# Kernel tuning notes

Measured on AMD Instinct MI355X. Metric: run time of the kernel, lower is better.

## Reference

```python
import jax, jax.numpy as jnp
import numpy as np

H = 1024      # hidden_dim
NH = 16       # num_heads
HD = H // NH  # head_dim
EPS = 1e-12
SCALE = float(np.sqrt(H))


def setup_inputs() -> dict:
    key = jax.random.key(0)
    ks = jax.random.split(key, 12)
    S, B = 2048, 2
    inp = {
        "query": jax.random.normal(ks[0], (S, B, 2 * H), jnp.float32),
        "key":   jax.random.normal(ks[1], (S, B, H), jnp.float32),
        "value": jax.random.normal(ks[2], (S, B, H), jnp.float32),
        # gating params (zeros in torch init, but randomize for a meaningful test)
        "qs": jax.random.normal(ks[3], (1, 1, H), jnp.float32) * 0.02,
        "ks_p": jax.random.normal(ks[4], (1, 1, H), jnp.float32) * 0.02,
        "vs": jax.random.normal(ks[5], (1, 1, H), jnp.float32) * 0.02,
        # Overparam vq: Linear(H, 2H)
        "vq_w": jax.random.normal(ks[6], (2 * H, H), jnp.float32) * (1.0 / np.sqrt(H)),
        "vq_b": jax.random.normal(ks[7], (2 * H,), jnp.float32) * 0.02,
        # q_linear: Linear(2H, H)
        "ql_w": jax.random.normal(ks[8], (H, 2 * H), jnp.float32) * (1.0 / np.sqrt(2 * H)),
        "ql_b": jax.random.normal(ks[9], (H,), jnp.float32) * 0.02,
        # LayerNorm(H)
        "ln_g": jnp.ones((H,), jnp.float32),
        "ln_b": jnp.zeros((H,), jnp.float32),
    }
    return inp


def _layernorm(x, g, b):
    mu = jnp.mean(x, axis=-1, keepdims=True)
    var = jnp.mean(jnp.square(x - mu), axis=-1, keepdims=True)
    return (x - mu) * jax.lax.rsqrt(var + EPS) * g + b


def reference(query, key, value, qs, ks_p, vs, vq_w, vq_b, ql_w, ql_b, ln_g, ln_b):
    # gate vectors
    qsig = jax.nn.sigmoid(qs)            # [1,1,H]
    ksig = jax.nn.sigmoid(ks_p)          # [1,1,H]
    # vq = Overparam(sigmoid(vs)): c,f = l1(x).split(H); sigmoid(f)*tanh(c)
    h = jax.nn.sigmoid(vs) @ vq_w.T + vq_b   # [1,1,2H]
    c, f = h[..., :H], h[..., H:]
    vsig = jax.nn.sigmoid(f) * jnp.tanh(c)   # [1,1,H]

    q = qsig * _layernorm(query @ ql_w.T + ql_b, ln_g, ln_b)  # [S,B,H]
    k = ksig * key
    v = vsig * value

    # batch-first
    q = jnp.transpose(q, (1, 0, 2))  # [B,Q,H]
    k = jnp.transpose(k, (1, 0, 2))  # [B,K,H]
    v = jnp.transpose(v, (1, 0, 2))
    B, Q, _ = q.shape
    K = k.shape[1]

    qh = q.reshape(B, Q, NH, HD)
    kh = k.reshape(B, K, NH, HD)
    vh = v.reshape(B, K, NH, HD)

    scores = jnp.einsum('bqhd,bkhd->bhqk', qh, kh) / SCALE
    w = jax.nn.softmax(scores, axis=-1)                # [B,NH,Q,K]
    out = jnp.einsum('bhqk,bkhd->bqhd', w, vh).reshape(B, Q, H)
    # torch code's final .transpose(0,1) is not assigned -> output is [Q,B,H]
    return jnp.transpose(out, (1, 0, 2))
```

## Files before the change

kernel.cpp:

```cpp
#include <hip/hip_runtime.h>

typedef __bf16 bf16x8 __attribute__((ext_vector_type(8)));
typedef float f32x4 __attribute__((ext_vector_type(4)));
typedef unsigned short u16x8 __attribute__((ext_vector_type(8)));
typedef unsigned short u16x4 __attribute__((ext_vector_type(4)));
typedef unsigned short u16;
typedef unsigned int u32;


__device__ __forceinline__ float b2f(u16 u) {
  union { unsigned int i; float f; } x; x.i = ((unsigned int)u) << 16; return x.f;
}
__device__ __forceinline__ u16 f2b(float f) {
  union { float f; unsigned int i; } x; x.f = f;
  unsigned int r = (x.i + 0x7fffu + ((x.i >> 16) & 1u)) >> 16;
  return (u16)r;
}
__device__ __forceinline__ float sigm(float x) { return 1.0f / (1.0f + __expf(-x)); }

__device__ __forceinline__ void async16(u16* lds, const u16* g) {
  __builtin_amdgcn_global_load_lds((const __attribute__((address_space(1))) void*)g,
                                   (__attribute__((address_space(3))) void*)lds, 16, 0, 0);
}

__global__ __launch_bounds__(256) void k_cvt_all(const float4* __restrict__ q, u16x4* __restrict__ qd,
                                                 const float4* __restrict__ w, u16x4* __restrict__ wd,
                                                 const float4* __restrict__ k, u16x4* __restrict__ kd,
                                                 const float4* __restrict__ v, u16x4* __restrict__ vd) {
  int b = blockIdx.x;
  const float4* s; u16x4* d; int i;
  if (b < 8192)       { s = q; d = qd; i = b * 256 + threadIdx.x; }
  else if (b < 10240) { s = w; d = wd; i = (b - 8192) * 256 + threadIdx.x; }
  else if (b < 14336) { s = k; d = kd; i = (b - 10240) * 256 + threadIdx.x; }
  else                { s = v; d = vd; i = (b - 14336) * 256 + threadIdx.x; }
  float4 x = s[i];
  u16x4 o; o[0] = f2b(x.x); o[1] = f2b(x.y); o[2] = f2b(x.z); o[3] = f2b(x.w);
  d[i] = o;
}

__global__ __launch_bounds__(256) void k_h(const float* __restrict__ vs,
                                           const float* __restrict__ vq_w,
                                           const float* __restrict__ vq_b,
                                           float* __restrict__ h) {
  __shared__ float svs[1024];
  int t = threadIdx.x;
  for (int i = t; i < 1024; i += 256) svs[i] = sigm(vs[i]);
  __syncthreads();
  int wave = t >> 6, lane = t & 63;
  int row = blockIdx.x * 4 + wave;
  const float4* w4 = (const float4*)(vq_w + (size_t)row * 1024);
  const float4* s4 = (const float4*)svs;
  float acc = 0.f;
#pragma unroll
  for (int k = 0; k < 4; ++k) {
    float4 w = w4[k * 64 + lane];
    float4 s = s4[k * 64 + lane];
    acc += w.x * s.x + w.y * s.y + w.z * s.z + w.w * s.w;
  }
#pragma unroll
  for (int off = 1; off < 64; off <<= 1) acc += __shfl_xor(acc, off);
  if (lane == 0) h[row] = acc + vq_b[row];
}

__global__ __launch_bounds__(256) void k_scales(const float* __restrict__ h,
                                                const float* __restrict__ qs,
                                                const float* __restrict__ ks,
                                                float* __restrict__ qk_scale,
                                                float* __restrict__ vsig) {
  int ch = blockIdx.x * 256 + threadIdx.x;
  qk_scale[ch] = sigm(qs[ch]) * sigm(ks[ch]) * (1.0f / 32.0f);
  float c = h[ch], f = h[1024 + ch];
  vsig[ch] = sigm(f) * tanhf(c);
}

__global__ __launch_bounds__(256) void k_gemm(const u16* __restrict__ A,
                                              const u16* __restrict__ Bt,
                                              u16* __restrict__ C) {
  __shared__ __align__(16) u16 As[128 * 32];
  __shared__ __align__(16) u16 Bs[128 * 32];
  int tid = threadIdx.x;
  int wave = tid >> 6, lane = tid & 63;
  int l15 = lane & 15, quad = lane >> 4;
  int bx = blockIdx.x & 255;
  int kh = blockIdx.x >> 8;
  int kofs = kh << 10;
  int m0 = (bx >> 3) * 128;
  int n0 = (bx & 7) * 128;
  int wm = (wave >> 1) * 64, wn = (wave & 1) * 64;
  f32x4 acc[4][4] = {};
  int c1 = tid, c2 = tid + 256;
  const u16* ga1 = A + (size_t)(m0 + (c1 >> 2)) * 2048 + kofs + (c1 & 3) * 8;
  const u16* ga2 = A + (size_t)(m0 + (c2 >> 2)) * 2048 + kofs + (c2 & 3) * 8;
  const u16* gb1 = Bt + (size_t)(n0 + (c1 >> 2)) * 2048 + kofs + (c1 & 3) * 8;
  const u16* gb2 = Bt + (size_t)(n0 + (c2 >> 2)) * 2048 + kofs + (c2 & 3) * 8;
  u16* lA1 = As + wave * 512;
  u16* lA2 = As + 2048 + wave * 512;
  u16* lB1 = Bs + wave * 512;
  u16* lB2 = Bs + 2048 + wave * 512;
  for (int kt = 0; kt < 32; ++kt) {
    async16(lA1, ga1); async16(lA2, ga2);
    async16(lB1, gb1); async16(lB2, gb2);
    ga1 += 32; ga2 += 32; gb1 += 32; gb2 += 32;
    __syncthreads();
    bf16x8 af[4], bfr[4];
#pragma unroll
    for (int mt = 0; mt < 4; ++mt)
      af[mt] = *(const bf16x8*)(As + (wm + mt * 16 + l15) * 32 + quad * 8);
#pragma unroll
    for (int nt = 0; nt < 4; ++nt)
      bfr[nt] = *(const bf16x8*)(Bs + (wn + nt * 16 + l15) * 32 + quad * 8);
#pragma unroll
    for (int mt = 0; mt < 4; ++mt)
#pragma unroll
      for (int nt = 0; nt < 4; ++nt)
        acc[mt][nt] = __builtin_amdgcn_mfma_f32_16x16x32_bf16(af[mt], bfr[nt], acc[mt][nt], 0, 0, 0);
    __syncthreads();
  }
  u16* Cp = C + (size_t)kh * 4096 * 1024;
#pragma unroll
  for (int mt = 0; mt < 4; ++mt) {
#pragma unroll
    for (int r = 0; r < 4; ++r) {
      int m = m0 + wm + mt * 16 + quad * 4 + r;
      u16* crow = Cp + (size_t)m * 1024 + n0 + wn + l15;
#pragma unroll
      for (int nt = 0; nt < 4; ++nt) crow[nt * 16] = f2b(acc[mt][nt][r]);
    }
  }
}

__global__ __launch_bounds__(256) void k_ln(const u16* __restrict__ qpre0,
                                            const u16* __restrict__ qpre1,
                                            const float* __restrict__ ql_b,
                                            const float* __restrict__ ln_g,
                                            const float* __restrict__ ln_b,
                                            const float* __restrict__ qk_scale,
                                            u16* __restrict__ qatt) {
  int row = blockIdx.x;
  int t = threadIdx.x;
  u16x4 a4 = *(const u16x4*)(qpre0 + (size_t)row * 1024 + t * 4);
  u16x4 b4 = *(const u16x4*)(qpre1 + (size_t)row * 1024 + t * 4);
  float v[4];
  float s = 0.f, ss = 0.f;
#pragma unroll
  for (int j = 0; j < 4; ++j) {
    v[j] = b2f(a4[j]) + b2f(b4[j]) + ql_b[t * 4 + j];
    s += v[j]; ss += v[j] * v[j];
  }
#pragma unroll
  for (int off = 1; off < 64; off <<= 1) { s += __shfl_xor(s, off); ss += __shfl_xor(ss, off); }
  __shared__ float red[8];
  int wv = t >> 6, ln = t & 63;
  if (ln == 0) { red[wv] = s; red[4 + wv] = ss; }
  __syncthreads();
  s = red[0] + red[1] + red[2] + red[3];
  ss = red[4] + red[5] + red[6] + red[7];
  float mu = s * (1.f / 1024.f);
  float rstd = rsqrtf(ss * (1.f / 1024.f) - mu * mu + 1e-12f);
  int sidx = row >> 1, b = row & 1;
  int ch0 = t * 4;
  int hh = ch0 >> 6, hd0 = ch0 & 63;
  u16* dst = qatt + ((size_t)(b * 16 + hh) * 2048 + sidx) * 64 + hd0;
#pragma unroll
  for (int j = 0; j < 4; ++j) {
    int ch = ch0 + j;
    float y = (v[j] - mu) * rstd * ln_g[ch] + ln_b[ch];
    dst[j] = f2b(y * qk_scale[ch]);
  }
}

__global__ __launch_bounds__(256, 4) void k_attn(const u16* __restrict__ qatt,
                                                 const u16* __restrict__ key,
                                                 const u16* __restrict__ value,
                                                 const float* __restrict__ vsig,
                                                 float* __restrict__ out) {
  int bh = blockIdx.x & 31;
  int qt = blockIdx.x >> 5;
  int b = bh >> 4, h = bh & 15;
  int tid = threadIdx.x, wave = tid >> 6, lane = tid & 63;
  int l15 = lane & 15, quad = lane >> 4;
  int q0 = qt * 64;

  __shared__ __align__(16) u16 Kt[64 * 72];
  __shared__ __align__(16) u16 Vt[2][64 * 72];
  __shared__ __align__(16) u16 Pb[4][16 * 72];

  const u16* qrow = qatt + ((size_t)bh * 2048 + q0 + wave * 16 + l15) * 64 + quad * 8;
  bf16x8 qf0 = *(const bf16x8*)qrow;
  bf16x8 qf1 = *(const bf16x8*)(qrow + 32);

  const u16* kb = key + (size_t)b * 1024 + (size_t)h * 64;
  const u16* vb = value + (size_t)b * 1024 + (size_t)h * 64;
  u16* Pw = Pb[wave];

  int p = lane & 31;
  int chalf = lane >> 5;
  int chbase = wave * 16 + chalf * 8;
  const u16* vsrc = vb + (size_t)2 * p * 2048 + chbase;

  int krow = wave * 16 + (lane >> 3);
  int kch  = (lane & 7) * 8;
  const u16* ksrc = kb + (size_t)krow * 2048 + kch;
  u16* kdst = Kt + krow * 72 + kch;

  {
    u16x8 k0 = *(const u16x8*)ksrc;
    u16x8 k1 = *(const u16x8*)(ksrc + (size_t)8 * 2048);
    *(u16x8*)kdst = k0;
    *(u16x8*)(kdst + 8 * 72) = k1;
    u16x8 va = *(const u16x8*)vsrc;
    u16x8 vbq = *(const u16x8*)(vsrc + 2048);
#pragma unroll
    for (int c = 0; c < 8; ++c) {
      u32 pk = (u32)va[c] | ((u32)vbq[c] << 16);
      *(u32*)(&Vt[0][(chbase + c) * 72 + 2 * p]) = pk;
    }
  }
  __syncthreads();

  f32x4 oacc[4] = {};
  float l_i[4] = {0.f, 0.f, 0.f, 0.f};

  for (int kt = 0; kt < 32; ++kt) {
    int cur = kt & 1;
    f32x4 sacc[4] = {};
#pragma unroll
    for (int nt = 0; nt < 4; ++nt) {
      const u16* kr = Kt + (nt * 16 + l15) * 72 + quad * 8;
      bf16x8 kfa = *(const bf16x8*)kr;
      bf16x8 kfb = *(const bf16x8*)(kr + 32);
      sacc[nt] = __builtin_amdgcn_mfma_f32_16x16x32_bf16(qf0, kfa, sacc[nt], 0, 0, 0);
      sacc[nt] = __builtin_amdgcn_mfma_f32_16x16x32_bf16(qf1, kfb, sacc[nt], 0, 0, 0);
    }
    u16x8 pk0, pk1, va, vbq;
    if (kt < 31) {
      const u16* ks2 = ksrc + (size_t)(kt + 1) * 64 * 2048;
      pk0 = *(const u16x8*)ks2;
      pk1 = *(const u16x8*)(ks2 + (size_t)8 * 2048);
      const u16* vs2 = vsrc + (size_t)(kt + 1) * 64 * 2048;
      va = *(const u16x8*)vs2;
      vbq = *(const u16x8*)(vs2 + 2048);
    }
#pragma unroll
    for (int r = 0; r < 4; ++r) {
      float p0 = __expf(sacc[0][r]);
      float p1 = __expf(sacc[1][r]);
      float p2 = __expf(sacc[2][r]);
      float p3 = __expf(sacc[3][r]);
      l_i[r] += (p0 + p1) + (p2 + p3);
      u16* prow = Pw + (quad * 4 + r) * 72 + l15;
      prow[0]  = f2b(p0);
      prow[16] = f2b(p1);
      prow[32] = f2b(p2);
      prow[48] = f2b(p3);
    }
    bf16x8 pf0 = *(const bf16x8*)(Pw + l15 * 72 + quad * 8);
    bf16x8 pf1 = *(const bf16x8*)(Pw + l15 * 72 + 32 + quad * 8);
    const u16* vt = Vt[cur];
#pragma unroll
    for (int nt = 0; nt < 4; ++nt) {
      int ch = nt * 16 + l15;
      bf16x8 vf0 = *(const bf16x8*)(vt + ch * 72 + quad * 8);
      bf16x8 vf1 = *(const bf16x8*)(vt + ch * 72 + 32 + quad * 8);
      oacc[nt] = __builtin_amdgcn_mfma_f32_16x16x32_bf16(pf0, vf0, oacc[nt], 0, 0, 0);
      oacc[nt] = __builtin_amdgcn_mfma_f32_16x16x32_bf16(pf1, vf1, oacc[nt], 0, 0, 0);
    }
    __syncthreads();
    if (kt < 31) {
      *(u16x8*)kdst = pk0;
      *(u16x8*)(kdst + 8 * 72) = pk1;
      u16* vd = Vt[cur ^ 1];
#pragma unroll
      for (int c = 0; c < 8; ++c) {
        u32 pk = (u32)va[c] | ((u32)vbq[c] << 16);
        *(u32*)(&vd[(chbase + c) * 72 + 2 * p]) = pk;
      }
    }
    __syncthreads();
  }
#pragma unroll
  for (int r = 0; r < 4; ++r) {
    float l = l_i[r];
    l += __shfl_xor(l, 1);
    l += __shfl_xor(l, 2);
    l += __shfl_xor(l, 4);
    l += __shfl_xor(l, 8);
    l_i[r] = l;
  }
#pragma unroll
  for (int r = 0; r < 4; ++r) {
    int sq = q0 + wave * 16 + quad * 4 + r;
    float inv = 1.0f / l_i[r];
    float* orow = out + ((size_t)sq * 2 + b) * 1024 + h * 64;
#pragma unroll
    for (int nt = 0; nt < 4; ++nt) {
      int ch = nt * 16 + l15;
      orow[ch] = oacc[nt][r] * inv * vsig[h * 64 + ch];
    }
  }
}

extern "C" void kernel_launch(void* const* d_in, const int* in_sizes, int n_in,
                              void* d_out, int out_size, void* d_ws, size_t ws_size,
                              hipStream_t stream) {
  (void)in_sizes; (void)n_in; (void)out_size; (void)ws_size;
  const float* query = (const float*)d_in[0];
  const float* key   = (const float*)d_in[1];
  const float* value = (const float*)d_in[2];
  const float* qs    = (const float*)d_in[3];
  const float* ksp   = (const float*)d_in[4];
  const float* vs    = (const float*)d_in[5];
  const float* vq_w  = (const float*)d_in[6];
  const float* vq_b  = (const float*)d_in[7];
  const float* ql_w  = (const float*)d_in[8];
  const float* ql_b  = (const float*)d_in[9];
  const float* ln_g  = (const float*)d_in[10];
  const float* ln_b  = (const float*)d_in[11];
  float* out = (float*)d_out;

  float* ws = (float*)d_ws;
  float* h        = ws;
  float* qk_scale = ws + 2048;
  float* vsig     = ws + 3072;
  u16* qpre  = (u16*)(ws + 4096);
  u16* qbf   = qpre + (size_t)2 * 4096 * 1024;
  u16* qatt  = qbf;
  u16* wbf   = qbf + (size_t)4096 * 2048;
  u16* kbf   = wbf + (size_t)1024 * 2048;
  u16* vbf   = kbf + (size_t)4096 * 1024;

  hipLaunchKernelGGL(k_cvt_all, dim3(18432), dim3(256), 0, stream,
                     (const float4*)query, (u16x4*)qbf,
                     (const float4*)ql_w,  (u16x4*)wbf,
                     (const float4*)key,   (u16x4*)kbf,
                     (const float4*)value, (u16x4*)vbf);
  hipLaunchKernelGGL(k_h,      dim3(512),  dim3(256), 0, stream, vs, vq_w, vq_b, h);
  hipLaunchKernelGGL(k_scales, dim3(4),    dim3(256), 0, stream, h, qs, ksp, qk_scale, vsig);
  hipLaunchKernelGGL(k_gemm,   dim3(512),  dim3(256), 0, stream, qbf, wbf, qpre);
  hipLaunchKernelGGL(k_ln,     dim3(4096), dim3(256), 0, stream, qpre, qpre + (size_t)4096 * 1024,
                     ql_b, ln_g, ln_b, qk_scale, qatt);
  hipLaunchKernelGGL(k_attn,   dim3(1024), dim3(256), 0, stream, qatt, kbf, vbf, vsig, out);
}
```

Measured before the change: 244.2 us.

## Double query tile per attention block, double-buffer K, use exp2, drop scales kernel

Each attention block now handles 128 query rows (two 16-row fragments per wave), so every K/V tile staged in LDS is reused across twice as many queries. The grid is halved and occupancy is lowered to 2 blocks per CU. K is now double-buffered, which removes one barrier per iteration, and the log2(e) factor is folded into the query gate so softmax can use the native exp2. The separate k_scales kernel is removed: gates are computed inline in k_ln and the value gate in the attention epilogue. This trades more registers, LDS and fewer blocks for fewer LDS loads, fewer barriers and one fewer launch.

```diff
diff --git a/kernel.cpp b/kernel.cpp
--- a/kernel.cpp
+++ b/kernel.cpp
@@ -7,6 +7,8 @@
 typedef unsigned short u16;
 typedef unsigned int u32;
 
+
+#define LOG2E 1.4426950408889634f
 
 __device__ __forceinline__ float b2f(u16 u) {
   union { unsigned int i; float f; } x; x.i = ((unsigned int)u) << 16; return x.f;
@@ -60,17 +62,6 @@
 #pragma unroll
   for (int off = 1; off < 64; off <<= 1) acc += __shfl_xor(acc, off);
   if (lane == 0) h[row] = acc + vq_b[row];
-}
-
-__global__ __launch_bounds__(256) void k_scales(const float* __restrict__ h,
-                                                const float* __restrict__ qs,
-                                                const float* __restrict__ ks,
-                                                float* __restrict__ qk_scale,
-                                                float* __restrict__ vsig) {
-  int ch = blockIdx.x * 256 + threadIdx.x;
-  qk_scale[ch] = sigm(qs[ch]) * sigm(ks[ch]) * (1.0f / 32.0f);
-  float c = h[ch], f = h[1024 + ch];
-  vsig[ch] = sigm(f) * tanhf(c);
 }
 
 __global__ __launch_bounds__(256) void k_gemm(const u16* __restrict__ A,
@@ -134,7 +125,8 @@
                                             const float* __restrict__ ql_b,
                                             const float* __restrict__ ln_g,
                                             const float* __restrict__ ln_b,
-                                            const float* __restrict__ qk_scale,
+                                            const float* __restrict__ qs,
+                                            const float* __restrict__ ks,
                                             u16* __restrict__ qatt) {
   int row = blockIdx.x;
   int t = threadIdx.x;
@@ -164,73 +156,80 @@
 #pragma unroll
   for (int j = 0; j < 4; ++j) {
     int ch = ch0 + j;
+    float gate = sigm(qs[ch]) * sigm(ks[ch]) * (LOG2E / 32.0f);
     float y = (v[j] - mu) * rstd * ln_g[ch] + ln_b[ch];
-    dst[j] = f2b(y * qk_scale[ch]);
-  }
-}
-
-__global__ __launch_bounds__(256, 4) void k_attn(const u16* __restrict__ qatt,
+    dst[j] = f2b(y * gate);
+  }
+}
+
+__global__ __launch_bounds__(256, 2) void k_attn(const u16* __restrict__ qatt,
                                                  const u16* __restrict__ key,
                                                  const u16* __restrict__ value,
-                                                 const float* __restrict__ vsig,
+                                                 const float* __restrict__ hbuf,
                                                  float* __restrict__ out) {
   int bh = blockIdx.x & 31;
   int qt = blockIdx.x >> 5;
   int b = bh >> 4, h = bh & 15;
   int tid = threadIdx.x, wave = tid >> 6, lane = tid & 63;
   int l15 = lane & 15, quad = lane >> 4;
-  int q0 = qt * 64;
-
-  __shared__ __align__(16) u16 Kt[64 * 72];
+  int q0 = qt * 128;
+
+  __shared__ __align__(16) u16 Kt[2][64 * 72];
   __shared__ __align__(16) u16 Vt[2][64 * 72];
-  __shared__ __align__(16) u16 Pb[4][16 * 72];
-
-  const u16* qrow = qatt + ((size_t)bh * 2048 + q0 + wave * 16 + l15) * 64 + quad * 8;
-  bf16x8 qf0 = *(const bf16x8*)qrow;
-  bf16x8 qf1 = *(const bf16x8*)(qrow + 32);
+  __shared__ __align__(16) u16 Pb[4][32 * 72];
+
+  bf16x8 qf[2][2];
+#pragma unroll
+  for (int f = 0; f < 2; ++f) {
+    const u16* qrow = qatt + ((size_t)bh * 2048 + q0 + f * 64 + wave * 16 + l15) * 64 + quad * 8;
+    qf[f][0] = *(const bf16x8*)qrow;
+    qf[f][1] = *(const bf16x8*)(qrow + 32);
+  }
 
   const u16* kb = key + (size_t)b * 1024 + (size_t)h * 64;
   const u16* vb = value + (size_t)b * 1024 + (size_t)h * 64;
   u16* Pw = Pb[wave];
 
   int p = lane & 31;
-  int chalf = lane >> 5;
-  int chbase = wave * 16 + chalf * 8;
+  int chbase = wave * 16 + (lane >> 5) * 8;
   const u16* vsrc = vb + (size_t)2 * p * 2048 + chbase;
-
   int krow = wave * 16 + (lane >> 3);
   int kch  = (lane & 7) * 8;
   const u16* ksrc = kb + (size_t)krow * 2048 + kch;
-  u16* kdst = Kt + krow * 72 + kch;
+  int kdofs = krow * 72 + kch;
+  int vdofs_base = 2 * p;
 
   {
     u16x8 k0 = *(const u16x8*)ksrc;
     u16x8 k1 = *(const u16x8*)(ksrc + (size_t)8 * 2048);
-    *(u16x8*)kdst = k0;
-    *(u16x8*)(kdst + 8 * 72) = k1;
+    *(u16x8*)(&Kt[0][kdofs]) = k0;
+    *(u16x8*)(&Kt[0][kdofs + 8 * 72]) = k1;
     u16x8 va = *(const u16x8*)vsrc;
     u16x8 vbq = *(const u16x8*)(vsrc + 2048);
 #pragma unroll
     for (int c = 0; c < 8; ++c) {
       u32 pk = (u32)va[c] | ((u32)vbq[c] << 16);
-      *(u32*)(&Vt[0][(chbase + c) * 72 + 2 * p]) = pk;
+      *(u32*)(&Vt[0][(chbase + c) * 72 + vdofs_base]) = pk;
     }
   }
   __syncthreads();
 
-  f32x4 oacc[4] = {};
-  float l_i[4] = {0.f, 0.f, 0.f, 0.f};
+  f32x4 oacc[2][4] = {};
+  float l_i[2][4] = {};
 
   for (int kt = 0; kt < 32; ++kt) {
     int cur = kt & 1;
-    f32x4 sacc[4] = {};
+    f32x4 sacc[2][4] = {};
+    const u16* ktc = Kt[cur];
 #pragma unroll
     for (int nt = 0; nt < 4; ++nt) {
-      const u16* kr = Kt + (nt * 16 + l15) * 72 + quad * 8;
+      const u16* kr = ktc + (nt * 16 + l15) * 72 + quad * 8;
       bf16x8 kfa = *(const bf16x8*)kr;
       bf16x8 kfb = *(const bf16x8*)(kr + 32);
-      sacc[nt] = __builtin_amdgcn_mfma_f32_16x16x32_bf16(qf0, kfa, sacc[nt], 0, 0, 0);
-      sacc[nt] = __builtin_amdgcn_mfma_f32_16x16x32_bf16(qf1, kfb, sacc[nt], 0, 0, 0);
+      sacc[0][nt] = __builtin_amdgcn_mfma_f32_16x16x32_bf16(qf[0][0], kfa, sacc[0][nt], 0, 0, 0);
+      sacc[0][nt] = __builtin_amdgcn_mfma_f32_16x16x32_bf16(qf[0][1], kfb, sacc[0][nt], 0, 0, 0);
+      sacc[1][nt] = __builtin_amdgcn_mfma_f32_16x16x32_bf16(qf[1][0], kfa, sacc[1][nt], 0, 0, 0);
+      sacc[1][nt] = __builtin_amdgcn_mfma_f32_16x16x32_bf16(qf[1][1], kfb, sacc[1][nt], 0, 0, 0);
     }
     u16x8 pk0, pk1, va, vbq;
     if (kt < 31) {
@@ -242,62 +241,79 @@
       vbq = *(const u16x8*)(vs2 + 2048);
     }
 #pragma unroll
-    for (int r = 0; r < 4; ++r) {
-      float p0 = __expf(sacc[0][r]);
-      float p1 = __expf(sacc[1][r]);
-      float p2 = __expf(sacc[2][r]);
-      float p3 = __expf(sacc[3][r]);
-      l_i[r] += (p0 + p1) + (p2 + p3);
-      u16* prow = Pw + (quad * 4 + r) * 72 + l15;
-      prow[0]  = f2b(p0);
-      prow[16] = f2b(p1);
-      prow[32] = f2b(p2);
-      prow[48] = f2b(p3);
-    }
-    bf16x8 pf0 = *(const bf16x8*)(Pw + l15 * 72 + quad * 8);
-    bf16x8 pf1 = *(const bf16x8*)(Pw + l15 * 72 + 32 + quad * 8);
+    for (int f = 0; f < 2; ++f) {
+#pragma unroll
+      for (int r = 0; r < 4; ++r) {
+        float p0 = __builtin_amdgcn_exp2f(sacc[f][0][r]);
+        float p1 = __builtin_amdgcn_exp2f(sacc[f][1][r]);
+        float p2 = __builtin_amdgcn_exp2f(sacc[f][2][r]);
+        float p3 = __builtin_amdgcn_exp2f(sacc[f][3][r]);
+        l_i[f][r] += (p0 + p1) + (p2 + p3);
+        u16* prow = Pw + (f * 16 + quad * 4 + r) * 72 + l15;
+        prow[0]  = f2b(p0);
+        prow[16] = f2b(p1);
+        prow[32] = f2b(p2);
+        prow[48] = f2b(p3);
+      }
+    }
+    bf16x8 pf[2][2];
+#pragma unroll
+    for (int f = 0; f < 2; ++f) {
+      pf[f][0] = *(const bf16x8*)(Pw + (f * 16 + l15) * 72 + quad * 8);
+      pf[f][1] = *(const bf16x8*)(Pw + (f * 16 + l15) * 72 + 32 + quad * 8);
+    }
     const u16* vt = Vt[cur];
 #pragma unroll
     for (int nt = 0; nt < 4; ++nt) {
-      int ch = nt * 16 + l15;
-      bf16x8 vf0 = *(const bf16x8*)(vt + ch * 72 + quad * 8);
-      bf16x8 vf1 = *(const bf16x8*)(vt + ch * 72 + 32 + quad * 8);
-      oacc[nt] = __builtin_amdgcn_mfma_f32_16x16x32_bf16(pf0, vf0, oacc[nt], 0, 0, 0);
-      oacc[nt] = __builtin_amdgcn_mfma_f32_16x16x32_bf16(pf1, vf1, oacc[nt], 0, 0, 0);
-    }
-    __syncthreads();
+      const u16* vr = vt + (nt * 16 + l15) * 72 + quad * 8;
+      bf16x8 vf0 = *(const bf16x8*)vr;
+      bf16x8 vf1 = *(const bf16x8*)(vr + 32);
+      oacc[0][nt] = __builtin_amdgcn_mfma_f32_16x16x32_bf16(pf[0][0], vf0, oacc[0][nt], 0, 0, 0);
+      oacc[0][nt] = __builtin_amdgcn_mfma_f32_16x16x32_bf16(pf[0][1], vf1, oacc[0][nt], 0, 0, 0);
+      oacc[1][nt] = __builtin_amdgcn_mfma_f32_16x16x32_bf16(pf[1][0], vf0, oacc[1][nt], 0, 0, 0);
+      oacc[1][nt] = __builtin_amdgcn_mfma_f32_16x16x32_bf16(pf[1][1], vf1, oacc[1][nt], 0, 0, 0);
+    }
     if (kt < 31) {
-      *(u16x8*)kdst = pk0;
-      *(u16x8*)(kdst + 8 * 72) = pk1;
+      u16* kd = Kt[cur ^ 1];
+      *(u16x8*)(&kd[kdofs]) = pk0;
+      *(u16x8*)(&kd[kdofs + 8 * 72]) = pk1;
       u16* vd = Vt[cur ^ 1];
 #pragma unroll
       for (int c = 0; c < 8; ++c) {
         u32 pk = (u32)va[c] | ((u32)vbq[c] << 16);
-        *(u32*)(&vd[(chbase + c) * 72 + 2 * p]) = pk;
+        *(u32*)(&vd[(chbase + c) * 72 + vdofs_base]) = pk;
       }
     }
     __syncthreads();
   }
 #pragma unroll
-  for (int r = 0; r < 4; ++r) {
-    float l = l_i[r];
-    l += __shfl_xor(l, 1);
-    l += __shfl_xor(l, 2);
-    l += __shfl_xor(l, 4);
-    l += __shfl_xor(l, 8);
-    l_i[r] = l;
-  }
-#pragma unroll
-  for (int r = 0; r < 4; ++r) {
-    int sq = q0 + wave * 16 + quad * 4 + r;
-    float inv = 1.0f / l_i[r];
-    float* orow = out + ((size_t)sq * 2 + b) * 1024 + h * 64;
-#pragma unroll
-    for (int nt = 0; nt < 4; ++nt) {
-      int ch = nt * 16 + l15;
-      orow[ch] = oacc[nt][r] * inv * vsig[h * 64 + ch];
-    }
-  }
+  for (int f = 0; f < 2; ++f)
+#pragma unroll
+    for (int r = 0; r < 4; ++r) {
+      float l = l_i[f][r];
+      l += __shfl_xor(l, 1);
+      l += __shfl_xor(l, 2);
+      l += __shfl_xor(l, 4);
+      l += __shfl_xor(l, 8);
+      l_i[f][r] = l;
+    }
+  float vsg[4];
+#pragma unroll
+  for (int nt = 0; nt < 4; ++nt) {
+    int ch = h * 64 + nt * 16 + l15;
+    vsg[nt] = sigm(hbuf[1024 + ch]) * tanhf(hbuf[ch]);
+  }
+#pragma unroll
+  for (int f = 0; f < 2; ++f)
+#pragma unroll
+    for (int r = 0; r < 4; ++r) {
+      int sq = q0 + f * 64 + wave * 16 + quad * 4 + r;
+      float inv = 1.0f / l_i[f][r];
+      float* orow = out + ((size_t)sq * 2 + b) * 1024 + h * 64;
+#pragma unroll
+      for (int nt = 0; nt < 4; ++nt)
+        orow[nt * 16 + l15] = oacc[f][nt][r] * inv * vsg[nt];
+    }
 }
 
 extern "C" void kernel_launch(void* const* d_in, const int* in_sizes, int n_in,
@@ -319,9 +335,7 @@
   float* out = (float*)d_out;
 
   float* ws = (float*)d_ws;
-  float* h        = ws;
-  float* qk_scale = ws + 2048;
-  float* vsig     = ws + 3072;
+  float* h   = ws;
   u16* qpre  = (u16*)(ws + 4096);
   u16* qbf   = qpre + (size_t)2 * 4096 * 1024;
   u16* qatt  = qbf;
@@ -334,10 +348,9 @@
                      (const float4*)ql_w,  (u16x4*)wbf,
                      (const float4*)key,   (u16x4*)kbf,
                      (const float4*)value, (u16x4*)vbf);
-  hipLaunchKernelGGL(k_h,      dim3(512),  dim3(256), 0, stream, vs, vq_w, vq_b, h);
-  hipLaunchKernelGGL(k_scales, dim3(4),    dim3(256), 0, stream, h, qs, ksp, qk_scale, vsig);
-  hipLaunchKernelGGL(k_gemm,   dim3(512),  dim3(256), 0, stream, qbf, wbf, qpre);
-  hipLaunchKernelGGL(k_ln,     dim3(4096), dim3(256), 0, stream, qpre, qpre + (size_t)4096 * 1024,
-                     ql_b, ln_g, ln_b, qk_scale, qatt);
-  hipLaunchKernelGGL(k_attn,   dim3(1024), dim3(256), 0, stream, qatt, kbf, vbf, vsig, out);
-}
+  hipLaunchKernelGGL(k_h,    dim3(512),  dim3(256), 0, stream, vs, vq_w, vq_b, h);
+  hipLaunchKernelGGL(k_gemm, dim3(512),  dim3(256), 0, stream, qbf, wbf, qpre);
+  hipLaunchKernelGGL(k_ln,   dim3(4096), dim3(256), 0, stream, qpre, qpre + (size_t)4096 * 1024,
+                     ql_b, ln_g, ln_b, qs, ksp, qatt);
+  hipLaunchKernelGGL(k_attn, dim3(512),  dim3(256), 0, stream, qatt, kbf, vbf, h, out);
+}
```

Measured after the change: 242.8 us. About the same (-0.5%).
